# Kernel optimization log

Hardware: AMD Instinct MI355X
Metric: run time of the kernel (lower is better)

The kernel has to match this reference:

```python
import jax, jax.numpy as jnp
import numpy as np

B, S, D, H = 2, 2048, 2048, 32
HD = D // H  # head_dim = 64
NEG = -1e10


def setup_inputs() -> dict:
    key = jax.random.key(0)
    k1, k2, k3 = jax.random.split(key, 3)
    hidden_states = jax.random.normal(k1, (B, S, D), dtype=jnp.float32)
    W = jax.random.normal(k2, (D, 3 * D), dtype=jnp.float32) * (1.0 / np.sqrt(D))
    b = jax.random.normal(k3, (3 * D,), dtype=jnp.float32) * 0.02
    return {"hidden_states": hidden_states, "W": W, "b": b}


def reference(hidden_states, W, b):
    # fused QKV projection: [B,S,D] @ [D,3D] -> [B,S,3D]
    qvk = hidden_states @ W + b
    # OPT interleaved layout: reshape to [B,S,D,3]; channel 0=q, 1=v, 2=k
    qvk = qvk.reshape(B, S, D, 3)
    q = qvk[..., 0].reshape(B, S, H, HD)
    v = qvk[..., 1].reshape(B, S, H, HD)
    k = qvk[..., 2].reshape(B, S, H, HD)
    # causal bias: -1e10 strictly above diagonal, shape [1,1,S,S]
    bias = jnp.triu(jnp.full((S, S), NEG, dtype=jnp.float32), 1)[None, None]
    # dot_product_attention_weights: scale q by 1/sqrt(head_dim)
    scale = jnp.asarray(1.0 / np.sqrt(HD), dtype=jnp.float32)
    scores = jnp.einsum('bqhd,bkhd->bhqk', q * scale, k) + bias  # [B,H,S,S]
    attn_weights = jax.nn.softmax(scores, axis=-1)
    attn_output = jnp.einsum('bhqk,bkhd->bqhd', attn_weights, v)  # [B,S,H,HD]
    return attn_output.reshape(B, S, D)
```

## Files before the change

### kernel.cpp

```cpp
#include <hip/hip_runtime.h>
#include <hip/hip_bf16.h>
#include <stdint.h>

typedef unsigned short ushort_t;
typedef __bf16 bf16x8 __attribute__((ext_vector_type(8)));
typedef float f32x4 __attribute__((ext_vector_type(4)));
typedef float f32x16 __attribute__((ext_vector_type(16)));
typedef int int4v __attribute__((ext_vector_type(4)));
typedef ushort_t ushort8 __attribute__((ext_vector_type(8)));

__device__ __forceinline__ ushort_t f2bf(float f) {
  union { float f; unsigned int u; } v; v.f = f;
  unsigned int r = v.u + 0x7fffu + ((v.u >> 16) & 1u);
  return (ushort_t)(r >> 16);
}

__device__ __forceinline__ bf16x8 ld_bf8(const ushort_t* p) {
  return *reinterpret_cast<const bf16x8*>(p);
}

__device__ __forceinline__ void g2lds16(const void* g, void* l) {
  __builtin_amdgcn_global_load_lds(
      (const __attribute__((address_space(1))) unsigned int*)g,
      (__attribute__((address_space(3))) unsigned int*)l,
      16, 0, 0);
}

__device__ __forceinline__ float ex2(float x) { return __builtin_amdgcn_exp2f(x); }

__device__ __forceinline__ int cvtpk(float a, float b) {
  int r;
  asm("v_cvt_pk_bf16_f32 %0, %1, %2" : "=v"(r) : "v"(a), "v"(b));
  return r;
}

__global__ __launch_bounds__(256) void cvt_hs(const float* __restrict__ in,
                                              ushort_t* __restrict__ out) {
  int i = (blockIdx.x * 256 + threadIdx.x) * 8;
  float4 a = *reinterpret_cast<const float4*>(in + i);
  float4 b = *reinterpret_cast<const float4*>(in + i + 4);
  ushort8 r;
  r[0] = f2bf(a.x); r[1] = f2bf(a.y); r[2] = f2bf(a.z); r[3] = f2bf(a.w);
  r[4] = f2bf(b.x); r[5] = f2bf(b.y); r[6] = f2bf(b.z); r[7] = f2bf(b.w);
  *reinterpret_cast<ushort8*>(out + i) = r;
}

__global__ __launch_bounds__(256) void transpose_W(const float* __restrict__ Win,
                                                   ushort_t* __restrict__ Wt) {
  __shared__ ushort_t T[64][65];
  const int t = threadIdx.x;
  const int k0 = (blockIdx.x & 31) * 64;
  const int n0 = (blockIdx.x >> 5) * 64;
#pragma unroll
  for (int i = 0; i < 16; ++i) {
    int idx = i * 256 + t;
    int r = idx >> 6, c = idx & 63;
    T[r][c] = f2bf(Win[(k0 + r) * 6144 + n0 + c]);
  }
  __syncthreads();
#pragma unroll
  for (int i = 0; i < 16; ++i) {
    int idx = i * 256 + t;
    int nr = idx >> 6, kc = idx & 63;
    Wt[(n0 + nr) * 2048 + k0 + kc] = T[kc][nr];
  }
}

__global__ __launch_bounds__(256, 2) void gemm_qkv(
    const ushort_t* __restrict__ A, const ushort_t* __restrict__ Bt,
    const float* __restrict__ bias,
    ushort_t* __restrict__ Qb, ushort_t* __restrict__ Kb,
    ushort_t* __restrict__ VT) {
  __shared__ __align__(16) char smem[40960];
  ushort_t* A0 = (ushort_t*)smem;
  ushort_t* A1 = (ushort_t*)(smem + 8192);
  ushort_t* B0 = (ushort_t*)(smem + 16384);
  ushort_t* B1 = (ushort_t*)(smem + 28672);
  ushort_t* Cs = (ushort_t*)smem;
  const int t = threadIdx.x;
  const int w = t >> 6, l = t & 63;
  const int lo = l & 15, hi = l >> 4;
  const int wr = w >> 1, wc = w & 1;

  int bid = blockIdx.x;
  int swz = (bid & 7) * 128 + (bid >> 3);
  const int mt = swz & 31, nt = swz >> 5;
  const int bm = mt * 128;
  const int bn = nt * 192;

  f32x4 acc[4][6];
#pragma unroll
  for (int i = 0; i < 4; ++i)
#pragma unroll
    for (int j = 0; j < 6; ++j) acc[i][j] = f32x4{0.f, 0.f, 0.f, 0.f};

  const ushort_t* Ag = A + (size_t)bm * 2048;
  const ushort_t* Bg = Bt + (size_t)bn * 2048;

#define STAGE(Ad, Bd, kk_)                                       \
  do {                                                           \
    for (int r2 = 0; r2 < 2; ++r2) {                             \
      int c_ = r2 * 256 + t;                                     \
      int row_ = c_ >> 2, s4_ = c_ & 3;                          \
      int slot_ = s4_ ^ ((row_ & 3) ^ ((row_ >> 2) & 3));        \
      g2lds16(Ag + row_ * 2048 + (kk_) + slot_ * 8, (Ad) + c_ * 8); \
    }                                                            \
    for (int r3 = 0; r3 < 3; ++r3) {                             \
      int c_ = r3 * 256 + t;                                     \
      int row_ = c_ >> 2, s4_ = c_ & 3;                          \
      int slot_ = s4_ ^ ((row_ & 3) ^ ((row_ >> 2) & 3));        \
      g2lds16(Bg + row_ * 2048 + (kk_) + slot_ * 8, (Bd) + c_ * 8); \
    }                                                            \
  } while (0)

  STAGE(A0, B0, 0);
  __syncthreads();
  ushort_t *Ac = A0, *Bc = B0, *An = A1, *Bn = B1;

  for (int kk = 0; kk < 2048; kk += 32) {
    if (kk + 32 < 2048) STAGE(An, Bn, kk + 32);
    bf16x8 af[4], bfr[6];
#pragma unroll
    for (int mf = 0; mf < 4; ++mf) {
      int row = wr * 64 + mf * 16 + lo;
      int fr = (row & 3) ^ ((row >> 2) & 3);
      af[mf] = ld_bf8(Ac + row * 32 + ((hi ^ fr) << 3));
    }
#pragma unroll
    for (int nf = 0; nf < 6; ++nf) {
      int row = wc * 96 + nf * 16 + lo;
      int fr = (row & 3) ^ ((row >> 2) & 3);
      bfr[nf] = ld_bf8(Bc + row * 32 + ((hi ^ fr) << 3));
    }
    __builtin_amdgcn_s_setprio(1);
#pragma unroll
    for (int mf = 0; mf < 4; ++mf)
#pragma unroll
      for (int nf = 0; nf < 6; ++nf)
        acc[mf][nf] = __builtin_amdgcn_mfma_f32_16x16x32_bf16(
            af[mf], bfr[nf], acc[mf][nf], 0, 0, 0);
    __builtin_amdgcn_s_setprio(0);
    __syncthreads();
    ushort_t* tmp;
    tmp = Ac; Ac = An; An = tmp;
    tmp = Bc; Bc = Bn; Bn = tmp;
  }
#undef STAGE

  float bv[6];
  int ch[6];
#pragma unroll
  for (int nf = 0; nf < 6; ++nf) {
    int nl = wc * 96 + nf * 16 + lo;
    bv[nf] = bias[bn + nl];
    ch[nf] = nl % 3;
  }
  const int b_ = bm >> 11;
  const int bh = (b_ << 5) + nt;
  const float QS = 0.125f * 1.44269504f;

#pragma unroll
  for (int h = 0; h < 2; ++h) {
    if (wr == h) {
#pragma unroll
      for (int mf = 0; mf < 4; ++mf)
#pragma unroll
        for (int nf = 0; nf < 6; ++nf) {
          int rloc = mf * 16 + hi * 4;
          int nl = wc * 96 + nf * 16 + lo;
          f32x4 a = acc[mf][nf];
#pragma unroll
          for (int j = 0; j < 4; ++j) {
            float v = a[j] + bv[nf];
            if (ch[nf] == 0) v *= QS;
            Cs[(rloc + j) * 200 + nl] = f2bf(v);
          }
        }
    }
    __syncthreads();
    const int sbase = (bm & 2047) + h * 64;
#pragma unroll
    for (int it = 0; it < 2; ++it) {
      int slot = it * 256 + t;
      int r = slot >> 3, g = slot & 7;
      ushort8 vq, vk;
#pragma unroll
      for (int u = 0; u < 8; ++u) {
        int hd = g * 8 + u;
        vq[u] = Cs[r * 200 + hd * 3];
        vk[u] = Cs[r * 200 + hd * 3 + 2];
      }
      size_t rowoff = ((size_t)bh * 2048 + sbase + r) * 64 + g * 8;
      *reinterpret_cast<ushort8*>(Qb + rowoff) = vq;
      *reinterpret_cast<ushort8*>(Kb + rowoff) = vk;
    }
#pragma unroll
    for (int it = 0; it < 2; ++it) {
      int slot = it * 256 + t;
      int hd = slot >> 3, sg = slot & 7;
      ushort8 vv;
#pragma unroll
      for (int u = 0; u < 8; ++u) vv[u] = Cs[(sg * 8 + u) * 200 + hd * 3 + 1];
      *reinterpret_cast<ushort8*>(VT + ((size_t)bh * 64 + hd) * 2048 + sbase +
                                  sg * 8) = vv;
    }
    __syncthreads();
  }
}

__device__ __forceinline__ void ldkv(const ushort_t* kp, const ushort_t* vp,
                                     bf16x8 k[4], bf16x8 v0[2], bf16x8 v1[2]) {
#pragma unroll
  for (int dc = 0; dc < 4; ++dc) k[dc] = ld_bf8(kp + dc * 16);
#pragma unroll
  for (int s = 0; s < 2; ++s) {
    v0[s] = ld_bf8(vp + s * 16);
    v1[s] = ld_bf8(vp + s * 16 + 32 * 2048);
  }
}

__device__ __forceinline__ void proc_chunk(const bf16x8 kf[4],
                                           const bf16x8 vf0[2],
                                           const bf16x8 vf1[2],
                                           const bf16x8 qf[4], f32x16& o0,
                                           f32x16& o1, float& mr, float& lr,
                                           bool diag, int ql, int hi) {
  f32x16 p;
#pragma unroll
  for (int r = 0; r < 16; ++r) p[r] = 0.f;
  __builtin_amdgcn_s_setprio(1);
#pragma unroll
  for (int dc = 0; dc < 4; ++dc)
    p = __builtin_amdgcn_mfma_f32_32x32x16_bf16(kf[dc], qf[dc], p, 0, 0, 0);
  __builtin_amdgcn_s_setprio(0);
  if (diag) {
#pragma unroll
    for (int r = 0; r < 16; ++r) {
      int kvr = (r & 3) + 8 * (r >> 2) + 4 * hi;
      if (kvr > ql) p[r] = -1e30f;
    }
  }
  float a0 = fmaxf(p[0], p[1]), a1 = fmaxf(p[2], p[3]);
  float a2 = fmaxf(p[4], p[5]), a3 = fmaxf(p[6], p[7]);
  float a4 = fmaxf(p[8], p[9]), a5 = fmaxf(p[10], p[11]);
  float a6 = fmaxf(p[12], p[13]), a7 = fmaxf(p[14], p[15]);
  float mx = fmaxf(fmaxf(fmaxf(a0, a1), fmaxf(a2, a3)),
                   fmaxf(fmaxf(a4, a5), fmaxf(a6, a7)));
  if (__any(mx > mr + 10.0f)) {
    mx = fmaxf(mx, __shfl_xor(mx, 32));
    float mn = fmaxf(mr, mx);
    float scl = ex2(mr - mn);
    mr = mn;
    lr *= scl;
#pragma unroll
    for (int r = 0; r < 16; ++r) { o0[r] *= scl; o1[r] *= scl; }
  }
#pragma unroll
  for (int r = 0; r < 16; ++r) p[r] = ex2(p[r] - mr);
  float s0 = (p[0] + p[1]) + (p[2] + p[3]);
  float s1 = (p[4] + p[5]) + (p[6] + p[7]);
  float s2 = (p[8] + p[9]) + (p[10] + p[11]);
  float s3 = (p[12] + p[13]) + (p[14] + p[15]);
  lr += (s0 + s1) + (s2 + s3);

  __builtin_amdgcn_s_setprio(1);
#pragma unroll
  for (int s = 0; s < 2; ++s) {
    int x0 = cvtpk(p[8 * s + 0], p[8 * s + 1]);
    int x1 = cvtpk(p[8 * s + 2], p[8 * s + 3]);
    int y0 = cvtpk(p[8 * s + 4], p[8 * s + 5]);
    int y1 = cvtpk(p[8 * s + 6], p[8 * s + 7]);
    int ox0 = __shfl_xor(x0, 32);
    int ox1 = __shfl_xor(x1, 32);
    int oy0 = __shfl_xor(y0, 32);
    int oy1 = __shfl_xor(y1, 32);
    int4v wv;
    wv[0] = hi ? oy0 : x0;
    wv[1] = hi ? oy1 : x1;
    wv[2] = hi ? y0 : ox0;
    wv[3] = hi ? y1 : ox1;
    bf16x8 pf = __builtin_bit_cast(bf16x8, wv);
    o0 = __builtin_amdgcn_mfma_f32_32x32x16_bf16(vf0[s], pf, o0, 0, 0, 0);
    o1 = __builtin_amdgcn_mfma_f32_32x32x16_bf16(vf1[s], pf, o1, 0, 0, 0);
  }
  __builtin_amdgcn_s_setprio(0);
}

__global__ __launch_bounds__(64) void attn(
    const ushort_t* __restrict__ Qb, const ushort_t* __restrict__ Kb,
    const ushort_t* __restrict__ VT, float* __restrict__ out) {
  __shared__ float Ld[32 * 66];
  const int l = threadIdx.x;
  const int ql = l & 31, hi = l >> 5;

  const int bid = blockIdx.x;
  const int bh = bid & 63;
  const int pr = bid >> 6;
  const int b_ = bh >> 5, h = bh & 31;

  const ushort_t* kbase = Kb + bh * 2048 * 64 + hi * 8;
  const ushort_t* vbase = VT + (bh * 64 + ql) * 2048 + hi * 8;
  const int KSTR = 32 * 64;
  const int VSTR = 32;

#pragma unroll 1
  for (int tile = 0; tile < 2; ++tile) {
    const int qt = tile ? (63 - pr) : pr;
    const int q0 = qt * 32;
    const int nch = qt + 1;

    const ushort_t* qp = Qb + (bh * 2048 + q0 + ql) * 64 + hi * 8;
    bf16x8 qf[4];
#pragma unroll
    for (int dc = 0; dc < 4; ++dc) qf[dc] = ld_bf8(qp + dc * 16);

    f32x16 o0, o1;
#pragma unroll
    for (int r = 0; r < 16; ++r) { o0[r] = 0.f; o1[r] = 0.f; }
    float mr = -1e30f, lr = 0.f;

    bf16x8 kA[4], vA0[2], vA1[2], kB[4], vB0[2], vB1[2];
    const ushort_t* kp = kbase + ql * 64;
    const ushort_t* vp = vbase;
    ldkv(kp, vp, kA, vA0, vA1);

    int c = 0;
    while (c + 2 <= nch) {
      kp += KSTR; vp += VSTR;
      ldkv(kp, vp, kB, vB0, vB1);
      proc_chunk(kA, vA0, vA1, qf, o0, o1, mr, lr, false, ql, hi);
      if (c + 2 < nch) {
        kp += KSTR; vp += VSTR;
        ldkv(kp, vp, kA, vA0, vA1);
      }
      proc_chunk(kB, vB0, vB1, qf, o0, o1, mr, lr, (c + 1 == nch - 1), ql, hi);
      c += 2;
    }
    if (c < nch) {
      proc_chunk(kA, vA0, vA1, qf, o0, o1, mr, lr, true, ql, hi);
    }

    const float lrf = lr + __shfl_xor(lr, 32);
    const float inv = 1.0f / lrf;
#pragma unroll
    for (int r = 0; r < 16; ++r) {
      int hdv = (r & 3) + 8 * (r >> 2) + 4 * hi;
      Ld[ql * 66 + hdv] = o0[r] * inv;
      Ld[ql * 66 + 32 + hdv] = o1[r] * inv;
    }
    __syncthreads();
    float* op = out + (size_t)(b_ * 2048 + q0) * 2048 + h * 64 + l;
#pragma unroll
    for (int i = 0; i < 32; ++i) {
      op[(size_t)i * 2048] = Ld[i * 66 + l];
    }
    __syncthreads();
  }
}

extern "C" void kernel_launch(void* const* d_in, const int* in_sizes, int n_in,
                              void* d_out, int out_size, void* d_ws,
                              size_t ws_size, hipStream_t stream) {
  (void)in_sizes; (void)n_in; (void)out_size; (void)ws_size;
  const float* hs = (const float*)d_in[0];
  const float* W = (const float*)d_in[1];
  const float* bias = (const float*)d_in[2];
  float* out = (float*)d_out;

  char* ws = (char*)d_ws;
  ushort_t* Abf = (ushort_t*)(ws);
  ushort_t* Wt = (ushort_t*)(ws + (16u << 20));
  ushort_t* Qb = (ushort_t*)(ws + (40u << 20));
  ushort_t* Kb = (ushort_t*)(ws + (56u << 20));
  ushort_t* VT = (ushort_t*)(ws + (72u << 20));

  hipLaunchKernelGGL(cvt_hs, dim3(4096), dim3(256), 0, stream, hs, Abf);
  hipLaunchKernelGGL(transpose_W, dim3(3072), dim3(256), 0, stream, W, Wt);
  hipLaunchKernelGGL(gemm_qkv, dim3(1024), dim3(256), 0, stream, Abf, Wt, bias,
                     Qb, Kb, VT);
  hipLaunchKernelGGL(attn, dim3(2048), dim3(64), 0, stream, Qb, Kb, VT, out);
}
```

Baseline: 258.2 us.

## Share K/V chunk loads between paired causal query tiles in one pass

The kernel previously processed its two paired query tiles (p and 63-p) one after another, streaming K/V twice. Now both tiles' Q fragments and accumulators stay live at once, and a single K/V stream is applied to tile B for every chunk and to tile A for chunks up to p. This is meant to cut redundant global K/V loads for the first tile. In exchange it doubles accumulator register use, which risks spills or lower occupancy, and tile A's work is serialized inside tile B's loop.

```diff
diff --git a/kernel.cpp b/kernel.cpp
--- a/kernel.cpp
+++ b/kernel.cpp
@@ -295,7 +295,10 @@
 
   const int bid = blockIdx.x;
   const int bh = bid & 63;
-  const int pr = bid >> 6;
+  const int p = bid >> 6;
+  const int nchB = 64 - p;
+  const int q0A = p * 32;
+  const int q0B = (63 - p) * 32;
   const int b_ = bh >> 5, h = bh & 31;
 
   const ushort_t* kbase = Kb + bh * 2048 * 64 + hi * 8;
@@ -303,50 +306,63 @@
   const int KSTR = 32 * 64;
   const int VSTR = 32;
 
+  bf16x8 qfA[4], qfB[4];
+  {
+    const ushort_t* qpA = Qb + (bh * 2048 + q0A + ql) * 64 + hi * 8;
+    const ushort_t* qpB = Qb + (bh * 2048 + q0B + ql) * 64 + hi * 8;
+#pragma unroll
+    for (int dc = 0; dc < 4; ++dc) {
+      qfA[dc] = ld_bf8(qpA + dc * 16);
+      qfB[dc] = ld_bf8(qpB + dc * 16);
+    }
+  }
+
+  f32x16 oA0, oA1, oB0, oB1;
+#pragma unroll
+  for (int r = 0; r < 16; ++r) {
+    oA0[r] = 0.f; oA1[r] = 0.f; oB0[r] = 0.f; oB1[r] = 0.f;
+  }
+  float mA = -1e30f, lA = 0.f, mB = -1e30f, lB = 0.f;
+
+  bf16x8 kX[4], vX0[2], vX1[2], kY[4], vY0[2], vY1[2];
+  const ushort_t* kp = kbase + ql * 64;
+  const ushort_t* vp = vbase;
+  ldkv(kp, vp, kX, vX0, vX1);
+
+  int c = 0;
+  while (c + 2 <= nchB) {
+    kp += KSTR; vp += VSTR;
+    ldkv(kp, vp, kY, vY0, vY1);
+    proc_chunk(kX, vX0, vX1, qfB, oB0, oB1, mB, lB, false, ql, hi);
+    if (c <= p)
+      proc_chunk(kX, vX0, vX1, qfA, oA0, oA1, mA, lA, (c == p), ql, hi);
+    if (c + 2 < nchB) {
+      kp += KSTR; vp += VSTR;
+      ldkv(kp, vp, kX, vX0, vX1);
+    }
+    proc_chunk(kY, vY0, vY1, qfB, oB0, oB1, mB, lB, (c + 1 == nchB - 1), ql,
+               hi);
+    if (c + 1 <= p)
+      proc_chunk(kY, vY0, vY1, qfA, oA0, oA1, mA, lA, (c + 1 == p), ql, hi);
+    c += 2;
+  }
+  if (c < nchB) {
+    proc_chunk(kX, vX0, vX1, qfB, oB0, oB1, mB, lB, true, ql, hi);
+    if (c <= p)
+      proc_chunk(kX, vX0, vX1, qfA, oA0, oA1, mA, lA, (c == p), ql, hi);
+  }
+
 #pragma unroll 1
   for (int tile = 0; tile < 2; ++tile) {
-    const int qt = tile ? (63 - pr) : pr;
-    const int q0 = qt * 32;
-    const int nch = qt + 1;
-
-    const ushort_t* qp = Qb + (bh * 2048 + q0 + ql) * 64 + hi * 8;
-    bf16x8 qf[4];
-#pragma unroll
-    for (int dc = 0; dc < 4; ++dc) qf[dc] = ld_bf8(qp + dc * 16);
-
-    f32x16 o0, o1;
-#pragma unroll
-    for (int r = 0; r < 16; ++r) { o0[r] = 0.f; o1[r] = 0.f; }
-    float mr = -1e30f, lr = 0.f;
-
-    bf16x8 kA[4], vA0[2], vA1[2], kB[4], vB0[2], vB1[2];
-    const ushort_t* kp = kbase + ql * 64;
-    const ushort_t* vp = vbase;
-    ldkv(kp, vp, kA, vA0, vA1);
-
-    int c = 0;
-    while (c + 2 <= nch) {
-      kp += KSTR; vp += VSTR;
-      ldkv(kp, vp, kB, vB0, vB1);
-      proc_chunk(kA, vA0, vA1, qf, o0, o1, mr, lr, false, ql, hi);
-      if (c + 2 < nch) {
-        kp += KSTR; vp += VSTR;
-        ldkv(kp, vp, kA, vA0, vA1);
-      }
-      proc_chunk(kB, vB0, vB1, qf, o0, o1, mr, lr, (c + 1 == nch - 1), ql, hi);
-      c += 2;
-    }
-    if (c < nch) {
-      proc_chunk(kA, vA0, vA1, qf, o0, o1, mr, lr, true, ql, hi);
-    }
-
+    const float lr = tile ? lB : lA;
     const float lrf = lr + __shfl_xor(lr, 32);
     const float inv = 1.0f / lrf;
+    const int q0 = tile ? q0B : q0A;
 #pragma unroll
     for (int r = 0; r < 16; ++r) {
       int hdv = (r & 3) + 8 * (r >> 2) + 4 * hi;
-      Ld[ql * 66 + hdv] = o0[r] * inv;
-      Ld[ql * 66 + 32 + hdv] = o1[r] * inv;
+      Ld[ql * 66 + hdv] = (tile ? oB0[r] : oA0[r]) * inv;
+      Ld[ql * 66 + 32 + hdv] = (tile ? oB1[r] : oA1[r]) * inv;
     }
     __syncthreads();
     float* op = out + (size_t)(b_ * 2048 + q0) * 2048 + h * 64 + l;
```

After: 242.5 us. 1.06x faster.
